# Kernel optimization log

Hardware: AMD Instinct MI355X
Metric: run time of the kernel (lower is better)

## Reference

```python
import jax, jax.numpy as jnp
import numpy as np

D_MODEL = 1024
N_HEADS = 16
HEAD_DIM = D_MODEL // N_HEADS


def setup_inputs() -> dict:
    key = jax.random.key(0)
    k1, k2, k3 = jax.random.split(key, 3)
    x = jax.random.normal(k1, (4, 2048, D_MODEL), dtype=jnp.float32)
    # nn.Linear(d_model, 3*d_model, bias=False): weight [3*d_model, d_model]
    w_qkv = jax.random.normal(k2, (3 * D_MODEL, D_MODEL), dtype=jnp.float32) / np.sqrt(D_MODEL)
    w_out = jax.random.normal(k3, (D_MODEL, D_MODEL), dtype=jnp.float32) / np.sqrt(D_MODEL)
    return {"x": x, "w_qkv": w_qkv, "w_out": w_out}


def reference(x, w_qkv, w_out):
    B, T, C = x.shape
    qkv = jnp.einsum('btc,fc->btf', x, w_qkv)  # [B,T,3C]
    q, k, v = jnp.split(qkv, 3, axis=-1)

    def heads(t):
        return t.reshape(B, T, N_HEADS, HEAD_DIM).transpose(0, 2, 1, 3)  # [B,H,T,D]

    q, k, v = heads(q), heads(k), heads(v)
    scale = 1.0 / np.sqrt(HEAD_DIM).astype(np.float32)
    attn = jnp.einsum('bhqd,bhkd->bhqk', q, k) * scale  # [B,H,T,T]
    causal = jnp.tril(jnp.ones((T, T), dtype=bool))
    attn = jnp.where(causal[None, None], attn, -jnp.inf)
    attn = jax.nn.softmax(attn, axis=-1)
    out = jnp.einsum('bhqk,bhkd->bhqd', attn, v)
    out = out.transpose(0, 2, 1, 3).reshape(B, T, C)
    return jnp.einsum('btc,fc->btf', out, w_out)
```

## Files before the change

kernel.cpp:

```cpp
#include <hip/hip_runtime.h>
#include <hip/hip_bf16.h>
#include <type_traits>


typedef __attribute__((ext_vector_type(8))) short bf16x8;
typedef __attribute__((ext_vector_type(4))) float f32x4;

#define LDS_AS(p) ((__attribute__((address_space(3))) void*)(p))
#define GLB_AS(p) ((const __attribute__((address_space(1))) void*)(p))

__global__ __launch_bounds__(256) void cvt3_f32_bf16(const float* __restrict__ a,
                                                     const float* __restrict__ b,
                                                     const float* __restrict__ c,
                                                     __hip_bfloat16* __restrict__ oa,
                                                     __hip_bfloat16* __restrict__ ob,
                                                     __hip_bfloat16* __restrict__ oc,
                                                     int na4, int nb4, int nc4) {
  int i = blockIdx.x * 256 + threadIdx.x;
  const float* in; __hip_bfloat16* out;
  if (i < na4) { in = a; out = oa; }
  else if (i < na4 + nb4) { in = b; out = ob; i -= na4; }
  else if (i < na4 + nb4 + nc4) { in = c; out = oc; i -= na4 + nb4; }
  else return;
  float4 v = reinterpret_cast<const float4*>(in)[i];
  __hip_bfloat16 b0 = __float2bfloat16(v.x);
  __hip_bfloat16 b1 = __float2bfloat16(v.y);
  __hip_bfloat16 b2 = __float2bfloat16(v.z);
  __hip_bfloat16 b3 = __float2bfloat16(v.w);
  ushort4 u;
  u.x = *reinterpret_cast<unsigned short*>(&b0);
  u.y = *reinterpret_cast<unsigned short*>(&b1);
  u.z = *reinterpret_cast<unsigned short*>(&b2);
  u.w = *reinterpret_cast<unsigned short*>(&b3);
  reinterpret_cast<ushort4*>(out)[i] = u;
}

__global__ __launch_bounds__(512, 1) void gemm_bt256(const __hip_bfloat16* __restrict__ A,
                                                     const __hip_bfloat16* __restrict__ B,
                                                     __hip_bfloat16* __restrict__ C,
                                                     int M, int N, int K) {
  __shared__ __hip_bfloat16 As[2][256 * 64];
  __shared__ __hip_bfloat16 Bs[2][256 * 64];
  const int tid = threadIdx.x;
  const int lane = tid & 63;
  const int wid = tid >> 6;
  const int l15 = lane & 15, l4 = lane >> 4;
  const int wr = wid >> 2;
  const int wc = wid & 3;
  const int m0 = blockIdx.x * 256, n0 = blockIdx.y * 256;
  const int NT = K >> 6;
  f32x4 acc[8][4] = {};

#define STAGE256(buf, kt)                                                            \
  do {                                                                               \
    _Pragma("unroll")                                                                \
    for (int i_ = 0; i_ < 4; ++i_) {                                                 \
      const int slot_ = i_ * 512 + tid;                                              \
      const int row_ = slot_ >> 3, c8_ = slot_ & 7;                                  \
      const int gc_ = (c8_ ^ (row_ & 7)) * 8;                                        \
      __builtin_amdgcn_global_load_lds(                                              \
          GLB_AS(A + (size_t)(m0 + row_) * K + (kt) + gc_),                          \
          LDS_AS((char*)As[buf] + slot_ * 16), 16, 0, 0);                            \
      __builtin_amdgcn_global_load_lds(                                              \
          GLB_AS(B + (size_t)(n0 + row_) * K + (kt) + gc_),                          \
          LDS_AS((char*)Bs[buf] + slot_ * 16), 16, 0, 0);                            \
    }                                                                                \
  } while (0)

  STAGE256(0, 0);
  if (NT > 1) STAGE256(1, 64);

  for (int t = 0; t < NT; ++t) {
    const int cur = t & 1;
    if (t < NT - 1) asm volatile("s_waitcnt vmcnt(8)" ::: "memory");
    else            asm volatile("s_waitcnt vmcnt(0)" ::: "memory");
    __builtin_amdgcn_s_barrier();
    asm volatile("" ::: "memory");

#pragma unroll
    for (int q = 0; q < 4; ++q) {
      const int mbase = wr * 128 + (q & 1) * 64;
      const int nbase = wc * 64 + (q >> 1) * 32;
      bf16x8 af[4][2], bfr[2][2];
#pragma unroll
      for (int mi = 0; mi < 4; ++mi)
#pragma unroll
        for (int kk = 0; kk < 2; ++kk) {
          const int r = mbase + mi * 16 + l15;
          af[mi][kk] = *reinterpret_cast<const bf16x8*>(
              &As[cur][r * 64 + (((kk * 4 + l4) ^ (r & 7)) * 8)]);
        }
#pragma unroll
      for (int nj = 0; nj < 2; ++nj)
#pragma unroll
        for (int kk = 0; kk < 2; ++kk) {
          const int r = nbase + nj * 16 + l15;
          bfr[nj][kk] = *reinterpret_cast<const bf16x8*>(
              &Bs[cur][r * 64 + (((kk * 4 + l4) ^ (r & 7)) * 8)]);
        }
      __builtin_amdgcn_s_setprio(1);
#pragma unroll
      for (int mi = 0; mi < 4; ++mi)
#pragma unroll
        for (int nj = 0; nj < 2; ++nj) {
          acc[(q & 1) * 4 + mi][(q >> 1) * 2 + nj] = __builtin_amdgcn_mfma_f32_16x16x32_bf16(
              af[mi][0], bfr[nj][0], acc[(q & 1) * 4 + mi][(q >> 1) * 2 + nj], 0, 0, 0);
          acc[(q & 1) * 4 + mi][(q >> 1) * 2 + nj] = __builtin_amdgcn_mfma_f32_16x16x32_bf16(
              af[mi][1], bfr[nj][1], acc[(q & 1) * 4 + mi][(q >> 1) * 2 + nj], 0, 0, 0);
        }
      __builtin_amdgcn_s_setprio(0);
    }
    asm volatile("" ::: "memory");
    __builtin_amdgcn_s_barrier();
    asm volatile("" ::: "memory");
    if (t + 2 < NT) STAGE256(cur, (t + 2) << 6);
  }
#undef STAGE256

#pragma unroll
  for (int mi = 0; mi < 8; ++mi)
#pragma unroll
    for (int ni = 0; ni < 4; ++ni)
#pragma unroll
      for (int j = 0; j < 4; ++j) {
        const int m = m0 + wr * 128 + mi * 16 + l4 * 4 + j;
        const int n = n0 + wc * 64 + ni * 16 + l15;
        C[(size_t)m * N + n] = __float2bfloat16(acc[mi][ni][j]);
      }
}

template <typename TOUT>
__global__ __launch_bounds__(256) void gemm_bt(const __hip_bfloat16* __restrict__ A,
                                               const __hip_bfloat16* __restrict__ B,
                                               TOUT* __restrict__ C,
                                               int M, int N, int K) {
  __shared__ __hip_bfloat16 As[2][128 * 64];
  __shared__ __hip_bfloat16 Bs[2][128 * 64];
  const int tid = threadIdx.x;
  const int lane = tid & 63;
  const int wid = tid >> 6;
  const int l15 = lane & 15, l4 = lane >> 4;
  const int m0 = blockIdx.x * 128, n0 = blockIdx.y * 128;
  const int wr = (wid >> 1) * 64;
  const int wc = (wid & 1) * 64;
  const int NT = K >> 6;
  f32x4 acc[4][4] = {};

#pragma unroll
  for (int i = 0; i < 4; ++i) {
    const int slot = i * 256 + tid;
    const int row = slot >> 3, c8 = slot & 7;
    __builtin_amdgcn_global_load_lds(GLB_AS(A + (size_t)(m0 + row) * K + c8 * 8),
                                     LDS_AS((char*)As[0] + slot * 16), 16, 0, 0);
    __builtin_amdgcn_global_load_lds(GLB_AS(B + (size_t)(n0 + row) * K + c8 * 8),
                                     LDS_AS((char*)Bs[0] + slot * 16), 16, 0, 0);
  }
  __syncthreads();

  int cur = 0;
  for (int t = 0; t < NT; ++t) {
    if (t + 1 < NT) {
      const int kt = (t + 1) << 6;
#pragma unroll
      for (int i = 0; i < 4; ++i) {
        const int slot = i * 256 + tid;
        const int row = slot >> 3, c8 = slot & 7;
        __builtin_amdgcn_global_load_lds(GLB_AS(A + (size_t)(m0 + row) * K + kt + c8 * 8),
                                         LDS_AS((char*)As[cur ^ 1] + slot * 16), 16, 0, 0);
        __builtin_amdgcn_global_load_lds(GLB_AS(B + (size_t)(n0 + row) * K + kt + c8 * 8),
                                         LDS_AS((char*)Bs[cur ^ 1] + slot * 16), 16, 0, 0);
      }
    }
#pragma unroll
    for (int kk = 0; kk < 2; ++kk) {
      bf16x8 af[4], bfr[4];
#pragma unroll
      for (int mi = 0; mi < 4; ++mi)
        af[mi] = *reinterpret_cast<const bf16x8*>(&As[cur][(wr + mi * 16 + l15) * 64 + kk * 32 + l4 * 8]);
#pragma unroll
      for (int ni = 0; ni < 4; ++ni)
        bfr[ni] = *reinterpret_cast<const bf16x8*>(&Bs[cur][(wc + ni * 16 + l15) * 64 + kk * 32 + l4 * 8]);
#pragma unroll
      for (int mi = 0; mi < 4; ++mi)
#pragma unroll
        for (int ni = 0; ni < 4; ++ni)
          acc[mi][ni] = __builtin_amdgcn_mfma_f32_16x16x32_bf16(af[mi], bfr[ni], acc[mi][ni], 0, 0, 0);
    }
    if (t + 1 < NT) __syncthreads();
    cur ^= 1;
  }
#pragma unroll
  for (int mi = 0; mi < 4; ++mi)
#pragma unroll
    for (int ni = 0; ni < 4; ++ni)
#pragma unroll
      for (int j = 0; j < 4; ++j) {
        const int m = m0 + wr + mi * 16 + l4 * 4 + j;
        const int n = n0 + wc + ni * 16 + l15;
        if constexpr (std::is_same<TOUT, float>::value)
          C[(size_t)m * N + n] = acc[mi][ni][j];
        else
          C[(size_t)m * N + n] = __float2bfloat16(acc[mi][ni][j]);
      }
}

__global__ __launch_bounds__(512, 2) void attn_causal(const __hip_bfloat16* __restrict__ qkv,
                                                      __hip_bfloat16* __restrict__ o) {
  constexpr int T = 2048, F = 3072, C = 1024;
  __shared__ __hip_bfloat16 Ks[2][64 * 72];
  __shared__ __hip_bfloat16 Vts[2][64 * 72];
  __shared__ __hip_bfloat16 Ps[8][16 * 72];
  const int tid = threadIdx.x;
  const int wid = tid >> 6, lane = tid & 63;
  const int l15 = lane & 15, l4 = lane >> 4;
  const int x = blockIdx.x, h = blockIdx.y, b = blockIdx.z;
  const int qt = (wid < 4) ? x : (7 - x);
  const int nt = 4 * (7 - x) + 4;
  const int tmax = 4 * qt + (wid & 3);
  const int hoff = h * 64;
  const __hip_bfloat16* base = qkv + (size_t)b * T * F;
  const int Q0 = qt * 256 + (wid & 3) * 64;

  constexpr float SC = 0.125f * 1.44269504088896f;

  bf16x8 aq[4][2];
#pragma unroll
  for (int f = 0; f < 4; ++f)
#pragma unroll
    for (int kk = 0; kk < 2; ++kk) {
      bf16x8 q = *reinterpret_cast<const bf16x8*>(base + (size_t)(Q0 + f * 16 + l15) * F + hoff + kk * 32 + l4 * 8);
#pragma unroll
      for (int e = 0; e < 8; ++e) {
        const unsigned short raw = (unsigned short)q[e];
        const float fv = __uint_as_float((unsigned)raw << 16) * SC;
        __hip_bfloat16 qs = __float2bfloat16(fv);
        q[e] = *reinterpret_cast<short*>(&qs);
      }
      aq[f][kk] = q;
    }

  f32x4 acc[4][4] = {};
  float mrun[4], lrun[4];
#pragma unroll
  for (int f = 0; f < 4; ++f) { mrun[f] = -1e30f; lrun[f] = 0.f; }

  const int sV = tid;
  const int sK = tid - 256;
  bf16x8 sreg0, sreg1;
  if (wid < 4) {
    const size_t vr = (size_t)(2 * (sV >> 3)) * F + hoff + 2 * C + (sV & 7) * 8;
    sreg0 = *reinterpret_cast<const bf16x8*>(base + vr);
    sreg1 = *reinterpret_cast<const bf16x8*>(base + vr + F);
  } else {
    sreg0 = *reinterpret_cast<const bf16x8*>(base + (size_t)(sK >> 3) * F + hoff + C + (sK & 7) * 8);
    sreg1 = *reinterpret_cast<const bf16x8*>(base + (size_t)(32 + (sK >> 3)) * F + hoff + C + (sK & 7) * 8);
  }

  for (int t = 0; t < nt; ++t) {
    const int cur = t & 1;
    if (wid < 4) {
      const unsigned short* a0 = reinterpret_cast<const unsigned short*>(&sreg0);
      const unsigned short* a1 = reinterpret_cast<const unsigned short*>(&sreg1);
      const int c8 = sV & 7, r2 = sV >> 3;
      unsigned pk[8], tw[8], pkr[8];
#pragma unroll
      for (int j = 0; j < 8; ++j) pk[j] = (unsigned)a0[j] | ((unsigned)a1[j] << 16);
#pragma unroll
      for (int j = 0; j < 8; ++j) tw[j] = (c8 & 4) ? pk[(j + 4) & 7] : pk[j];
#pragma unroll
      for (int j = 0; j < 8; ++j) pkr[j] = (c8 & 2) ? tw[(j + 2) & 7] : tw[j];
#pragma unroll
      for (int j = 0; j < 8; ++j) tw[j] = (c8 & 1) ? pkr[(j + 1) & 7] : pkr[j];
#pragma unroll
      for (int jj = 0; jj < 8; ++jj) {
        const int d = c8 * 8 + ((jj + c8) & 7);
        *reinterpret_cast<unsigned*>(&Vts[cur][d * 72 + 2 * r2]) = tw[jj];
      }
    } else {
      *reinterpret_cast<bf16x8*>(&Ks[cur][(sK >> 3) * 72 + (sK & 7) * 8]) = sreg0;
      *reinterpret_cast<bf16x8*>(&Ks[cur][(32 + (sK >> 3)) * 72 + (sK & 7) * 8]) = sreg1;
    }
    __syncthreads();
    if (t + 1 < nt) {
      const int kn = (t + 1) * 64;
      if (wid < 4) {
        const size_t vr = (size_t)(kn + 2 * (sV >> 3)) * F + hoff + 2 * C + (sV & 7) * 8;
        sreg0 = *reinterpret_cast<const bf16x8*>(base + vr);
        sreg1 = *reinterpret_cast<const bf16x8*>(base + vr + F);
      } else {
        sreg0 = *reinterpret_cast<const bf16x8*>(base + (size_t)(kn + (sK >> 3)) * F + hoff + C + (sK & 7) * 8);
        sreg1 = *reinterpret_cast<const bf16x8*>(base + (size_t)(kn + 32 + (sK >> 3)) * F + hoff + C + (sK & 7) * 8);
      }
    }
    if (t > tmax) continue;
    const bool diag = (t == tmax);

    bf16x8 kf[4][2], vf[4][2];
#pragma unroll
    for (int kt = 0; kt < 4; ++kt)
#pragma unroll
      for (int kk = 0; kk < 2; ++kk)
        kf[kt][kk] = *reinterpret_cast<const bf16x8*>(&Ks[cur][(kt * 16 + l15) * 72 + kk * 32 + l4 * 8]);
#pragma unroll
    for (int di = 0; di < 4; ++di)
#pragma unroll
      for (int kk = 0; kk < 2; ++kk)
        vf[di][kk] = *reinterpret_cast<const bf16x8*>(&Vts[cur][(di * 16 + l15) * 72 + kk * 32 + l4 * 8]);

    __hip_bfloat16* pw = Ps[wid];
#pragma unroll
    for (int f = 0; f < 4; ++f) {
      f32x4 s[4];
#pragma unroll
      for (int kt = 0; kt < 4; ++kt) {
        f32x4 z = {};
        z = __builtin_amdgcn_mfma_f32_16x16x32_bf16(kf[kt][0], aq[f][0], z, 0, 0, 0);
        z = __builtin_amdgcn_mfma_f32_16x16x32_bf16(kf[kt][1], aq[f][1], z, 0, 0, 0);
        s[kt] = z;
      }
      if (diag) {
        const int ql = f * 16 + l15;
#pragma unroll
        for (int kt = 0; kt < 4; ++kt)
#pragma unroll
          for (int j = 0; j < 4; ++j) {
            const int kvl = kt * 16 + l4 * 4 + j;
            s[kt][j] = (kvl <= ql) ? s[kt][j] : -1e30f;
          }
      }

      float t0 = fmaxf(fmaxf(s[0][0], s[0][1]), s[0][2]);
      float t1 = fmaxf(fmaxf(s[0][3], s[1][0]), s[1][1]);
      float t2 = fmaxf(fmaxf(s[1][2], s[1][3]), s[2][0]);
      float t3 = fmaxf(fmaxf(s[2][1], s[2][2]), s[2][3]);
      float t4 = fmaxf(fmaxf(s[3][0], s[3][1]), s[3][2]);
      float mt = fmaxf(fmaxf(fmaxf(t0, t1), fmaxf(t2, t3)), fmaxf(t4, s[3][3]));
      mt = fmaxf(mt, __shfl_xor(mt, 16, 64));
      mt = fmaxf(mt, __shfl_xor(mt, 32, 64));
      const bool defer = __all(mt <= mrun[f] + 8.f);
      const float mnew = defer ? mrun[f] : fmaxf(mrun[f], mt);
      float rs = 0.f;
#pragma unroll
      for (int kt = 0; kt < 4; ++kt) {
        float p0 = exp2f(s[kt][0] - mnew), p1 = exp2f(s[kt][1] - mnew);
        float p2 = exp2f(s[kt][2] - mnew), p3 = exp2f(s[kt][3] - mnew);
        s[kt][0] = p0; s[kt][1] = p1; s[kt][2] = p2; s[kt][3] = p3;
        rs += (p0 + p1) + (p2 + p3);
      }
      rs += __shfl_xor(rs, 16, 64);
      rs += __shfl_xor(rs, 32, 64);
      if (defer) {
        lrun[f] += rs;
      } else {
        const float sco = exp2f(mrun[f] - mnew);
        lrun[f] = lrun[f] * sco + rs;
        mrun[f] = mnew;
#pragma unroll
        for (int di = 0; di < 4; ++di) acc[f][di] *= sco;
      }

#pragma unroll
      for (int kt = 0; kt < 4; ++kt) {
        unsigned w0, w1;
        asm("v_cvt_pk_bf16_f32 %0, %1, %2" : "=v"(w0) : "v"(s[kt][0]), "v"(s[kt][1]));
        asm("v_cvt_pk_bf16_f32 %0, %1, %2" : "=v"(w1) : "v"(s[kt][2]), "v"(s[kt][3]));
        unsigned long long dw = (unsigned long long)w0 | ((unsigned long long)w1 << 32);
        *reinterpret_cast<unsigned long long*>(&pw[l15 * 72 + kt * 16 + l4 * 4]) = dw;
      }
      asm volatile("s_waitcnt lgkmcnt(0)" ::: "memory");
      bf16x8 pa0 = *reinterpret_cast<const bf16x8*>(pw + l15 * 72 + l4 * 8);
      bf16x8 pa1 = *reinterpret_cast<const bf16x8*>(pw + l15 * 72 + 32 + l4 * 8);

#pragma unroll
      for (int di = 0; di < 4; ++di) {
        acc[f][di] = __builtin_amdgcn_mfma_f32_16x16x32_bf16(vf[di][0], pa0, acc[f][di], 0, 0, 0);
        acc[f][di] = __builtin_amdgcn_mfma_f32_16x16x32_bf16(vf[di][1], pa1, acc[f][di], 0, 0, 0);
      }
    }
  }

#pragma unroll
  for (int f = 0; f < 4; ++f) {
    const float inv = 1.0f / lrun[f];
    __hip_bfloat16* op = o + (size_t)((size_t)b * T + Q0 + f * 16 + l15) * C + hoff;
#pragma unroll
    for (int di = 0; di < 4; ++di) {
      ushort4 u;
      __hip_bfloat16 e0 = __float2bfloat16(acc[f][di][0] * inv);
      __hip_bfloat16 e1 = __float2bfloat16(acc[f][di][1] * inv);
      __hip_bfloat16 e2 = __float2bfloat16(acc[f][di][2] * inv);
      __hip_bfloat16 e3 = __float2bfloat16(acc[f][di][3] * inv);
      u.x = *reinterpret_cast<unsigned short*>(&e0);
      u.y = *reinterpret_cast<unsigned short*>(&e1);
      u.z = *reinterpret_cast<unsigned short*>(&e2);
      u.w = *reinterpret_cast<unsigned short*>(&e3);
      *reinterpret_cast<ushort4*>(op + di * 16 + l4 * 4) = u;
    }
  }
}

extern "C" void kernel_launch(void* const* d_in, const int* in_sizes, int n_in,
                              void* d_out, int out_size, void* d_ws, size_t ws_size,
                              hipStream_t stream) {
  const float* x = (const float*)d_in[0];
  const float* w_qkv = (const float*)d_in[1];
  const float* w_out = (const float*)d_in[2];
  float* out = (float*)d_out;

  constexpr int B = 4, T = 2048, C = 1024, F = 3 * C;
  constexpr int M = B * T;

  __hip_bfloat16* xb = (__hip_bfloat16*)d_ws;
  __hip_bfloat16* wqkvb = xb + (size_t)M * C;
  __hip_bfloat16* woutb = wqkvb + (size_t)F * C;
  __hip_bfloat16* qkvb = woutb + (size_t)C * C;
  __hip_bfloat16* attnb = qkvb + (size_t)M * F;

  constexpr int na4 = M * C / 4, nb4 = F * C / 4, nc4 = C * C / 4;
  cvt3_f32_bf16<<<(na4 + nb4 + nc4 + 255) / 256, 256, 0, stream>>>(
      x, w_qkv, w_out, xb, wqkvb, woutb, na4, nb4, nc4);

  gemm_bt256<<<dim3(M / 256, F / 256), 512, 0, stream>>>(xb, wqkvb, qkvb, M, F, C);

  attn_causal<<<dim3(4, 16, B), 512, 0, stream>>>(qkvb, attnb);

  gemm_bt<float><<<dim3(M / 128, C / 128), 256, 0, stream>>>(attnb, woutb, out, M, C, C);
}
```

Before: 221.7 us.

## Use 256x128 swizzled triple-stage output GEMM and grid-stride convert kernel

The output projection GEMM moves from 128x128 tiles with 4 waves to 256x128 tiles with 8 waves. It adds XOR-swizzled LDS layout to avoid bank conflicts, prefetches two stages ahead with vmcnt waits, and raises wave priority around the MFMA blocks. The fp32-to-bf16 convert kernel becomes a grid-stride loop with a fixed 2048-block grid. The larger tile launches fewer workgroups (256), which may reduce occupancy and CU balance in exchange for more data reuse.

```diff
diff --git a/kernel.cpp b/kernel.cpp
--- a/kernel.cpp
+++ b/kernel.cpp
@@ -16,23 +16,25 @@
                                                      __hip_bfloat16* __restrict__ ob,
                                                      __hip_bfloat16* __restrict__ oc,
                                                      int na4, int nb4, int nc4) {
-  int i = blockIdx.x * 256 + threadIdx.x;
-  const float* in; __hip_bfloat16* out;
-  if (i < na4) { in = a; out = oa; }
-  else if (i < na4 + nb4) { in = b; out = ob; i -= na4; }
-  else if (i < na4 + nb4 + nc4) { in = c; out = oc; i -= na4 + nb4; }
-  else return;
-  float4 v = reinterpret_cast<const float4*>(in)[i];
-  __hip_bfloat16 b0 = __float2bfloat16(v.x);
-  __hip_bfloat16 b1 = __float2bfloat16(v.y);
-  __hip_bfloat16 b2 = __float2bfloat16(v.z);
-  __hip_bfloat16 b3 = __float2bfloat16(v.w);
-  ushort4 u;
-  u.x = *reinterpret_cast<unsigned short*>(&b0);
-  u.y = *reinterpret_cast<unsigned short*>(&b1);
-  u.z = *reinterpret_cast<unsigned short*>(&b2);
-  u.w = *reinterpret_cast<unsigned short*>(&b3);
-  reinterpret_cast<ushort4*>(out)[i] = u;
+  const int ntot = na4 + nb4 + nc4;
+  for (int i = blockIdx.x * 256 + threadIdx.x; i < ntot; i += gridDim.x * 256) {
+    int j = i;
+    const float* in; __hip_bfloat16* out;
+    if (j < na4) { in = a; out = oa; }
+    else if (j < na4 + nb4) { in = b; out = ob; j -= na4; }
+    else { in = c; out = oc; j -= na4 + nb4; }
+    float4 v = reinterpret_cast<const float4*>(in)[j];
+    __hip_bfloat16 b0 = __float2bfloat16(v.x);
+    __hip_bfloat16 b1 = __float2bfloat16(v.y);
+    __hip_bfloat16 b2 = __float2bfloat16(v.z);
+    __hip_bfloat16 b3 = __float2bfloat16(v.w);
+    ushort4 u;
+    u.x = *reinterpret_cast<unsigned short*>(&b0);
+    u.y = *reinterpret_cast<unsigned short*>(&b1);
+    u.z = *reinterpret_cast<unsigned short*>(&b2);
+    u.w = *reinterpret_cast<unsigned short*>(&b3);
+    reinterpret_cast<ushort4*>(out)[j] = u;
+  }
 }
 
 __global__ __launch_bounds__(512, 1) void gemm_bt256(const __hip_bfloat16* __restrict__ A,
@@ -129,66 +131,84 @@
       }
 }
 
-template <typename TOUT>
-__global__ __launch_bounds__(256) void gemm_bt(const __hip_bfloat16* __restrict__ A,
-                                               const __hip_bfloat16* __restrict__ B,
-                                               TOUT* __restrict__ C,
-                                               int M, int N, int K) {
-  __shared__ __hip_bfloat16 As[2][128 * 64];
+__global__ __launch_bounds__(512, 1) void gemm_bt256x128f(const __hip_bfloat16* __restrict__ A,
+                                                          const __hip_bfloat16* __restrict__ B,
+                                                          float* __restrict__ C,
+                                                          int M, int N, int K) {
+  __shared__ __hip_bfloat16 As[2][256 * 64];
   __shared__ __hip_bfloat16 Bs[2][128 * 64];
   const int tid = threadIdx.x;
   const int lane = tid & 63;
   const int wid = tid >> 6;
   const int l15 = lane & 15, l4 = lane >> 4;
-  const int m0 = blockIdx.x * 128, n0 = blockIdx.y * 128;
   const int wr = (wid >> 1) * 64;
   const int wc = (wid & 1) * 64;
+  const int m0 = blockIdx.x * 256, n0 = blockIdx.y * 128;
   const int NT = K >> 6;
   f32x4 acc[4][4] = {};
 
-#pragma unroll
-  for (int i = 0; i < 4; ++i) {
-    const int slot = i * 256 + tid;
-    const int row = slot >> 3, c8 = slot & 7;
-    __builtin_amdgcn_global_load_lds(GLB_AS(A + (size_t)(m0 + row) * K + c8 * 8),
-                                     LDS_AS((char*)As[0] + slot * 16), 16, 0, 0);
-    __builtin_amdgcn_global_load_lds(GLB_AS(B + (size_t)(n0 + row) * K + c8 * 8),
-                                     LDS_AS((char*)Bs[0] + slot * 16), 16, 0, 0);
-  }
-  __syncthreads();
-
-  int cur = 0;
+#define STAGE2(buf, kt)                                                              \
+  do {                                                                               \
+    _Pragma("unroll")                                                                \
+    for (int i_ = 0; i_ < 4; ++i_) {                                                 \
+      const int slot_ = i_ * 512 + tid;                                              \
+      const int row_ = slot_ >> 3, c8_ = slot_ & 7;                                  \
+      const int gc_ = (c8_ ^ (row_ & 7)) * 8;                                        \
+      __builtin_amdgcn_global_load_lds(                                              \
+          GLB_AS(A + (size_t)(m0 + row_) * K + (kt) + gc_),                          \
+          LDS_AS((char*)As[buf] + slot_ * 16), 16, 0, 0);                            \
+    }                                                                                \
+    _Pragma("unroll")                                                                \
+    for (int i_ = 0; i_ < 2; ++i_) {                                                 \
+      const int slot_ = i_ * 512 + tid;                                              \
+      const int row_ = slot_ >> 3, c8_ = slot_ & 7;                                  \
+      const int gc_ = (c8_ ^ (row_ & 7)) * 8;                                        \
+      __builtin_amdgcn_global_load_lds(                                              \
+          GLB_AS(B + (size_t)(n0 + row_) * K + (kt) + gc_),                          \
+          LDS_AS((char*)Bs[buf] + slot_ * 16), 16, 0, 0);                            \
+    }                                                                                \
+  } while (0)
+
+  STAGE2(0, 0);
+  if (NT > 1) STAGE2(1, 64);
+
   for (int t = 0; t < NT; ++t) {
-    if (t + 1 < NT) {
-      const int kt = (t + 1) << 6;
-#pragma unroll
-      for (int i = 0; i < 4; ++i) {
-        const int slot = i * 256 + tid;
-        const int row = slot >> 3, c8 = slot & 7;
-        __builtin_amdgcn_global_load_lds(GLB_AS(A + (size_t)(m0 + row) * K + kt + c8 * 8),
-                                         LDS_AS((char*)As[cur ^ 1] + slot * 16), 16, 0, 0);
-        __builtin_amdgcn_global_load_lds(GLB_AS(B + (size_t)(n0 + row) * K + kt + c8 * 8),
-                                         LDS_AS((char*)Bs[cur ^ 1] + slot * 16), 16, 0, 0);
-      }
-    }
+    const int cur = t & 1;
+    if (t < NT - 1) asm volatile("s_waitcnt vmcnt(6)" ::: "memory");
+    else            asm volatile("s_waitcnt vmcnt(0)" ::: "memory");
+    __builtin_amdgcn_s_barrier();
+    asm volatile("" ::: "memory");
+
 #pragma unroll
     for (int kk = 0; kk < 2; ++kk) {
       bf16x8 af[4], bfr[4];
 #pragma unroll
-      for (int mi = 0; mi < 4; ++mi)
-        af[mi] = *reinterpret_cast<const bf16x8*>(&As[cur][(wr + mi * 16 + l15) * 64 + kk * 32 + l4 * 8]);
-#pragma unroll
-      for (int ni = 0; ni < 4; ++ni)
-        bfr[ni] = *reinterpret_cast<const bf16x8*>(&Bs[cur][(wc + ni * 16 + l15) * 64 + kk * 32 + l4 * 8]);
+      for (int mi = 0; mi < 4; ++mi) {
+        const int r = wr + mi * 16 + l15;
+        af[mi] = *reinterpret_cast<const bf16x8*>(
+            &As[cur][r * 64 + (((kk * 4 + l4) ^ (r & 7)) * 8)]);
+      }
+#pragma unroll
+      for (int ni = 0; ni < 4; ++ni) {
+        const int r = wc + ni * 16 + l15;
+        bfr[ni] = *reinterpret_cast<const bf16x8*>(
+            &Bs[cur][r * 64 + (((kk * 4 + l4) ^ (r & 7)) * 8)]);
+      }
+      __builtin_amdgcn_s_setprio(1);
 #pragma unroll
       for (int mi = 0; mi < 4; ++mi)
 #pragma unroll
         for (int ni = 0; ni < 4; ++ni)
           acc[mi][ni] = __builtin_amdgcn_mfma_f32_16x16x32_bf16(af[mi], bfr[ni], acc[mi][ni], 0, 0, 0);
-    }
-    if (t + 1 < NT) __syncthreads();
-    cur ^= 1;
-  }
+      __builtin_amdgcn_s_setprio(0);
+    }
+    asm volatile("" ::: "memory");
+    __builtin_amdgcn_s_barrier();
+    asm volatile("" ::: "memory");
+    if (t + 2 < NT) STAGE2(cur, (t + 2) << 6);
+  }
+#undef STAGE2
+
 #pragma unroll
   for (int mi = 0; mi < 4; ++mi)
 #pragma unroll
@@ -197,10 +217,7 @@
       for (int j = 0; j < 4; ++j) {
         const int m = m0 + wr + mi * 16 + l4 * 4 + j;
         const int n = n0 + wc + ni * 16 + l15;
-        if constexpr (std::is_same<TOUT, float>::value)
-          C[(size_t)m * N + n] = acc[mi][ni][j];
-        else
-          C[(size_t)m * N + n] = __float2bfloat16(acc[mi][ni][j]);
+        C[(size_t)m * N + n] = acc[mi][ni][j];
       }
 }
 
@@ -417,12 +434,11 @@
   __hip_bfloat16* attnb = qkvb + (size_t)M * F;
 
   constexpr int na4 = M * C / 4, nb4 = F * C / 4, nc4 = C * C / 4;
-  cvt3_f32_bf16<<<(na4 + nb4 + nc4 + 255) / 256, 256, 0, stream>>>(
-      x, w_qkv, w_out, xb, wqkvb, woutb, na4, nb4, nc4);
+  cvt3_f32_bf16<<<2048, 256, 0, stream>>>(x, w_qkv, w_out, xb, wqkvb, woutb, na4, nb4, nc4);
 
   gemm_bt256<<<dim3(M / 256, F / 256), 512, 0, stream>>>(xb, wqkvb, qkvb, M, F, C);
 
   attn_causal<<<dim3(4, 16, B), 512, 0, stream>>>(qkvb, attnb);
 
-  gemm_bt<float><<<dim3(M / 128, C / 128), 256, 0, stream>>>(attnb, woutb, out, M, C, C);
+  gemm_bt256x128f<<<dim3(M / 256, C / 128), 512, 0, stream>>>(attnb, woutb, out, M, C, C);
 }
```

Result: no change. 219.6 us (-1.0%).
